# Performance work log

Measured on AMD Instinct MI355X. Metric: run time of the kernel, lower is better.

The kernel has to match this reference:

```python
import jax, jax.numpy as jnp
import numpy as np

N, T, D, H, NH, BS = 4, 4096, 512, 8, 4, 64
DH = D // H                 # head dim = 64
NB = T // BS                # n_buckets = 64
CS = NH * NB                # chunk_size = 256
L = NH * T                  # sorted sequence length per head


def setup_inputs() -> dict:
    key = jax.random.key(0)
    ks = jax.random.split(key, 4)
    x = jax.random.normal(ks[0], (N, T, D), jnp.float32)
    W_Q = jax.random.normal(ks[1], (D, D), jnp.float32) * (D ** -0.5)
    W_V = jax.random.normal(ks[2], (D, D), jnp.float32) * (D ** -0.5)
    b_Q = jnp.zeros((D,), jnp.float32)
    b_V = jnp.zeros((D,), jnp.float32)
    gamma = jnp.ones((D,), jnp.float32)
    beta = jnp.zeros((D,), jnp.float32)
    # per-head random rotations: (dim_head, num_hashes, n_buckets // 2)
    rotations = jax.random.normal(ks[3], (H, DH, NH, NB // 2), jnp.float32)
    return {"x": x, "W_Q": W_Q, "b_Q": b_Q, "W_V": W_V, "b_V": b_V,
            "gamma": gamma, "beta": beta, "rotations": rotations}


def _look_one_back(a):
    # concat each chunk with the previous chunk (wrap-around for chunk 0)
    extra = jnp.concatenate([a[:, -1:], a[:, :-1]], axis=1)
    return jnp.concatenate([a, extra], axis=2)


def _lsh_head(qk, v, rot):
    # qk, v: [N, T, DH]; rot: [DH, NH, NB//2]
    rotated = jnp.einsum('btf,fhi->bhti', qk, rot)               # [N,NH,T,NB//2]
    rotated = jnp.concatenate([rotated, -rotated], axis=-1)       # [N,NH,T,NB]
    buckets = jnp.argmax(rotated, axis=-1)                        # [N,NH,T]
    offsets = (jnp.arange(NH) * NB)[None, :, None]
    buckets = (buckets + offsets).reshape(N, L)                   # [N, NH*T]

    ticker = jnp.broadcast_to(jnp.arange(L)[None, :], (N, L))
    buckets_and_t = T * buckets + (ticker % T)                    # unique keys
    sticker = jnp.argsort(buckets_and_t, axis=-1)                 # sorted ticker ids
    undo_sort = jnp.argsort(sticker, axis=-1)
    st = sticker % T                                              # original positions

    sqk = jnp.take_along_axis(qk, st[..., None], axis=1)          # [N,L,DH]
    sv = jnp.take_along_axis(v, st[..., None], axis=1)

    bq_t = st.reshape(N, CS, -1)                                  # [N,CS,BS]
    bqk = sqk.reshape(N, CS, -1, DH)
    bv = sv.reshape(N, CS, -1, DH)
    bq = bqk
    bk = bqk / (jnp.linalg.norm(bqk, axis=-1, keepdims=True) + 1e-6)

    bk = _look_one_back(bk)                                       # [N,CS,2*BS,DH]
    bv = _look_one_back(bv)
    bkv_t = _look_one_back(bq_t)

    dots = jnp.einsum('bcie,bcje->bcij', bq, bk) * (DH ** -0.5)   # [N,CS,BS,2BS]

    # mask out pairs hashed to different buckets
    q_sb = jnp.take_along_axis(buckets, sticker, axis=1).reshape(N, CS, -1)
    kv_sb = _look_one_back(q_sb)
    dots = jnp.where(q_sb[:, :, :, None] != kv_sb[:, :, None, :], -1e9, dots)
    # down-weight self-attention (same position)
    dots = jnp.where(bq_t[:, :, :, None] == bkv_t[:, :, None, :], -1e-5, dots)

    lse = jax.nn.logsumexp(dots, axis=-1, keepdims=True)
    probs = jnp.exp(dots - lse)
    bo = jnp.einsum('bcij,bcje->bcie', probs, bv)                 # [N,CS,BS,DH]

    so = bo.reshape(N, L, DH)
    slog = lse.reshape(N, L)
    o = jnp.take_along_axis(so, undo_sort[..., None], axis=1)
    logits = jnp.take_along_axis(slog, undo_sort, axis=1)

    o = o.reshape(N, NH, T, DH)
    logits = logits.reshape(N, NH, T, 1)
    pw = jnp.exp(logits - jax.nn.logsumexp(logits, axis=1, keepdims=True))
    return jnp.sum(o * pw, axis=1)                                # [N,T,DH]


def reference(x, W_Q, b_Q, W_V, b_V, gamma, beta, rotations):
    Q = x @ W_Q + b_Q
    V = x @ W_V + b_V
    Qh = Q.reshape(N, T, H, DH).transpose(2, 0, 1, 3)             # [H,N,T,DH]
    Vh = V.reshape(N, T, H, DH).transpose(2, 0, 1, 3)
    outs = jax.vmap(_lsh_head)(Qh, Vh, rotations)                 # [H,N,T,DH]
    out = outs.transpose(1, 2, 0, 3).reshape(N, T, D)
    mu = out.mean(axis=-1, keepdims=True)
    var = out.var(axis=-1, keepdims=True)
    return gamma * (out - mu) / jnp.sqrt(var + 1e-3) + beta
```

## Files before the change

kernel.cpp:

```cpp
#include <hip/hip_runtime.h>
#include <hip/hip_bf16.h>

#define N_ 4
#define T_ 4096
#define D_ 512
#define H_ 8
#define DH_ 64
#define NH_ 4
#define NB_ 64
#define CS_ 256
#define L_ 16384

typedef unsigned short u16;
typedef unsigned int u32;
typedef __attribute__((ext_vector_type(8))) short short8;
typedef __attribute__((ext_vector_type(8))) _Float16 half8;
typedef __attribute__((ext_vector_type(4))) float f32x4;

__device__ __forceinline__ u16 f2bf(float x){
    union { float f; u32 u; } c; c.f = x;
    u32 u = c.u;
    u32 r = (u + 0x7FFFu + ((u >> 16) & 1u)) >> 16;
    return (u16)r;
}
__device__ __forceinline__ float bf2f(u16 b){
    union { u32 u; float f; } c; c.u = ((u32)b) << 16;
    return c.f;
}
__device__ __forceinline__ u16 f2h(float x){
    _Float16 h = (_Float16)x;
    u16 r; __builtin_memcpy(&r, &h, 2); return r;
}

__global__ __launch_bounds__(256) void k_decXf(const float* __restrict__ x,
        u16* __restrict__ xf){
    int i = blockIdx.x * 256 + threadIdx.x;
    float4 v = ((const float4*)x)[i];
    ushort4 o;
    o.x = f2h(v.x); o.y = f2h(v.y); o.z = f2h(v.z); o.w = f2h(v.w);
    ((ushort4*)xf)[i] = o;
}

__global__ __launch_bounds__(256) void k_decWv(const float* __restrict__ Wv,
        u16* __restrict__ wvt){
    __shared__ float tile[32][33];
    const int tid = threadIdx.x;
    const int kt = blockIdx.x * 32, nt = blockIdx.y * 32;
    const int tx = tid & 31, ty = tid >> 5;
    #pragma unroll
    for (int i = 0; i < 4; ++i)
        tile[ty + i * 8][tx] = Wv[(size_t)(kt + ty + i * 8) * 512 + nt + tx];
    __syncthreads();
    #pragma unroll
    for (int i = 0; i < 4; ++i){
        int n = ty + i * 8;
        wvt[(size_t)(nt + n) * 512 + kt + tx] = f2h(tile[tx][n]);
    }
}

__global__ __launch_bounds__(256) void k_q(const float* __restrict__ x,
        const float* __restrict__ Wq, const float* __restrict__ bq,
        float* __restrict__ Q){
    __shared__ float sA[16][132];
    __shared__ float sB[16][68];
    const int tid = threadIdx.x;
    const int tx = tid & 15, ty = tid >> 4;
    const int mb = blockIdx.x * 128, nb = blockIdx.y * 64;
    float acc[8][4] = {};
    for (int k0 = 0; k0 < 512; k0 += 16){
        #pragma unroll
        for (int i = 0; i < 2; ++i){
            int idx = i * 256 + tid;
            int m = idx >> 2, kq = idx & 3;
            float4 v = *(const float4*)&x[(size_t)(mb + m) * 512 + k0 + kq * 4];
            sA[kq * 4 + 0][m] = v.x;
            sA[kq * 4 + 1][m] = v.y;
            sA[kq * 4 + 2][m] = v.z;
            sA[kq * 4 + 3][m] = v.w;
        }
        {
            int kk = tid >> 4, nq = tid & 15;
            *(float4*)&sB[kk][nq * 4] =
                *(const float4*)&Wq[(size_t)(k0 + kk) * 512 + nb + nq * 4];
        }
        __syncthreads();
        #pragma unroll
        for (int kk = 0; kk < 16; ++kk){
            float a[8], b[4];
            *(float4*)&a[0] = *(const float4*)&sA[kk][ty * 8];
            *(float4*)&a[4] = *(const float4*)&sA[kk][ty * 8 + 4];
            *(float4*)&b[0] = *(const float4*)&sB[kk][tx * 4];
            #pragma unroll
            for (int i = 0; i < 8; ++i)
                #pragma unroll
                for (int j = 0; j < 4; ++j) acc[i][j] += a[i] * b[j];
        }
        __syncthreads();
    }
    float4 bi = *(const float4*)&bq[nb + tx * 4];
    #pragma unroll
    for (int i = 0; i < 8; ++i){
        float4 o;
        o.x = acc[i][0] + bi.x; o.y = acc[i][1] + bi.y;
        o.z = acc[i][2] + bi.z; o.w = acc[i][3] + bi.w;
        *(float4*)&Q[(size_t)(mb + ty * 8 + i) * 512 + nb + tx * 4] = o;
    }
}

__global__ __launch_bounds__(256) void k_gemmV(const u16* __restrict__ xf,
        const u16* __restrict__ wvt, const float* __restrict__ bv,
        float* __restrict__ V){
    __shared__ __align__(16) u16 sA[128 * 40];
    __shared__ __align__(16) u16 sB[128 * 40];
    const int tid = threadIdx.x;
    const int mb = blockIdx.x * 128, nb = blockIdx.y * 128;
    const int w = tid >> 6, lane = tid & 63, quad = lane >> 4, cc = lane & 15;
    const int wm = (w & 1) * 64, wn = (w >> 1) * 64;
    f32x4 acc[4][4];
    #pragma unroll
    for (int i = 0; i < 4; ++i)
        #pragma unroll
        for (int j = 0; j < 4; ++j) acc[i][j] = (f32x4){0.f, 0.f, 0.f, 0.f};

    for (int k0 = 0; k0 < 512; k0 += 32){
        #pragma unroll
        for (int i = 0; i < 2; ++i){
            int idx = i * 256 + tid;
            int m = idx >> 2, ks = idx & 3;
            *(short8*)&sA[m * 40 + ks * 8] =
                *(const short8*)&xf[(size_t)(mb + m) * 512 + k0 + ks * 8];
            *(short8*)&sB[m * 40 + ks * 8] =
                *(const short8*)&wvt[(size_t)(nb + m) * 512 + k0 + ks * 8];
        }
        __syncthreads();
        half8 a[4], b[4];
        #pragma unroll
        for (int i = 0; i < 4; ++i){
            a[i] = *(const half8*)&sA[(wm + i * 16 + cc) * 40 + quad * 8];
            b[i] = *(const half8*)&sB[(wn + i * 16 + cc) * 40 + quad * 8];
        }
        #pragma unroll
        for (int i = 0; i < 4; ++i)
            #pragma unroll
            for (int j = 0; j < 4; ++j)
                acc[i][j] = __builtin_amdgcn_mfma_f32_16x16x32_f16(a[i], b[j], acc[i][j], 0, 0, 0);
        __syncthreads();
    }
    #pragma unroll
    for (int i = 0; i < 4; ++i)
        #pragma unroll
        for (int j = 0; j < 4; ++j){
            int c = nb + wn + j * 16 + cc;
            float bi = bv[c];
            #pragma unroll
            for (int r = 0; r < 4; ++r){
                int m = mb + wm + i * 16 + quad * 4 + r;
                V[(size_t)m * 512 + c] = acc[i][j][r] + bi;
            }
        }
}

__global__ __launch_bounds__(256) void k_rot(const float* __restrict__ Q,
        const float* __restrict__ rot, int* __restrict__ buckets){
    const int tb = blockIdx.x * 32;
    const int n = blockIdx.y, h = blockIdx.z;
    const int hn = h * N_ + n;
    __shared__ float Rs[64 * 128];
    __shared__ float Qs[32][64];
    const int tid = threadIdx.x;
    const float* rh = rot + (size_t)h * (64 * 128);
    for (int i = tid; i < 8192; i += 256) Rs[i] = rh[i];
    for (int i = tid; i < 2048; i += 256){
        int t = i >> 6, f = i & 63;
        Qs[t][f] = Q[(size_t)(n * T_ + tb + t) * 512 + h * 64 + f];
    }
    __syncthreads();
    const int tx = tid & 31, tg = tid >> 5;
    float r[4][4] = {};
    for (int f = 0; f < 64; ++f){
        float q0 = Qs[tg * 4 + 0][f], q1 = Qs[tg * 4 + 1][f];
        float q2 = Qs[tg * 4 + 2][f], q3 = Qs[tg * 4 + 3][f];
        #pragma unroll
        for (int jj = 0; jj < 4; ++jj){
            float rv = Rs[f * 128 + jj * 32 + tx];
            r[0][jj] += q0 * rv; r[1][jj] += q1 * rv;
            r[2][jj] += q2 * rv; r[3][jj] += q3 * rv;
        }
    }
    #pragma unroll
    for (int tt = 0; tt < 4; ++tt){
        #pragma unroll
        for (int jj = 0; jj < 4; ++jj){
            float bv = r[tt][jj]; int bi = tx;
            float nv = -bv;
            if (nv > bv){ bv = nv; bi = 32 + tx; }
            #pragma unroll
            for (int m = 16; m >= 1; m >>= 1){
                float ov = __shfl_xor(bv, m, 32);
                int   oi = __shfl_xor(bi, m, 32);
                if (ov > bv || (ov == bv && oi < bi)){ bv = ov; bi = oi; }
            }
            if (tx == 0){
                int t = tb + tg * 4 + tt;
                buckets[(size_t)hn * L_ + jj * T_ + t] = bi + jj * 64;
            }
        }
    }
}

__global__ __launch_bounds__(256) void k_hist(const int* __restrict__ buckets,
        int* __restrict__ hist){
    const int tile = blockIdx.x, hn = blockIdx.y;
    const int tid = threadIdx.x;
    __shared__ int h[256];
    h[tid] = 0;
    __syncthreads();
    int b = buckets[(size_t)hn * L_ + tile * 256 + tid];
    atomicAdd(&h[b], 1);
    __syncthreads();
    hist[((size_t)hn * 64 + tile) * 256 + tid] = h[tid];
}

__global__ __launch_bounds__(256) void k_scan(int* __restrict__ hist,
        int* __restrict__ bucketStart){
    const int hn = blockIdx.x;
    const int b = threadIdx.x;
    int* hh = hist + (size_t)hn * 64 * 256;
    int run = 0;
    for (int tl = 0; tl < 64; ++tl){
        int v = hh[tl * 256 + b];
        hh[tl * 256 + b] = run;
        run += v;
    }
    __shared__ int s[256];
    s[b] = run;
    __syncthreads();
    for (int off = 1; off < 256; off <<= 1){
        int add = (b >= off) ? s[b - off] : 0;
        __syncthreads();
        s[b] += add;
        __syncthreads();
    }
    bucketStart[hn * 256 + b] = s[b] - run;
}

__global__ __launch_bounds__(256) void k_scatter(const int* __restrict__ buckets,
        const int* __restrict__ offs, const int* __restrict__ bucketStart,
        int* __restrict__ sticker){
    const int tile = blockIdx.x, hn = blockIdx.y;
    const int tid = threadIdx.x;
    __shared__ int sb[256];
    const int i = tile * 256 + tid;
    const int b = buckets[(size_t)hn * L_ + i];
    sb[tid] = b;
    __syncthreads();
    int rank = 0;
    #pragma unroll 8
    for (int j = 0; j < 256; ++j){
        int v = sb[j];
        rank += (j < tid && v == b) ? 1 : 0;
    }
    int pos = bucketStart[hn * 256 + b]
            + offs[((size_t)hn * 64 + tile) * 256 + b]
            + rank;
    sticker[(size_t)hn * L_ + pos] = i;
}

__global__ __launch_bounds__(256) void k_attn(const float* __restrict__ Q,
        const float* __restrict__ V, const int* __restrict__ buckets,
        const int* __restrict__ sticker, u16* __restrict__ o_hash,
        float* __restrict__ logit_hash){
    const int blk_c = blockIdx.x, n = blockIdx.y, h = blockIdx.z;
    const int hn = h * N_ + n;
    const int tid = threadIdx.x;
    const int w = tid >> 6, lane = tid & 63;
    const int quad = lane >> 4, cc = lane & 15;

    __shared__ __align__(16) u16 sQ[128 * 64];
    __shared__ __align__(16) u16 sVt[64 * 128];
    __shared__ __align__(16) u16 sP[64 * 128];
    __shared__ int s_idx[128], s_buck[128], s_t[128];
    __shared__ float s_inv[128];
    __shared__ float s_lse[64];

    if (tid < 128){
        int cprev = (blk_c + CS_ - 1) & (CS_ - 1);
        int pos = (tid < 64) ? blk_c * 64 + tid : cprev * 64 + (tid - 64);
        int idx = sticker[(size_t)hn * L_ + pos];
        s_idx[tid] = idx;
        s_buck[tid] = buckets[(size_t)hn * L_ + idx];
        s_t[tid] = idx & (T_ - 1);
    }
    __syncthreads();

    for (int pass = 0; pass < 8; ++pass){
        int r = pass * 16 + w * 4 + quad;
        int t = s_t[r];
        const float4* qp = (const float4*)&Q[(size_t)(n * T_ + t) * 512 + h * 64];
        float4 qv = qp[cc];
        int c0 = cc * 4;
        int physq = ((c0 >> 3) ^ (r & 7));
        u16* dst = &sQ[r * 64 + physq * 8 + (c0 & 7)];
        dst[0] = f2bf(qv.x); dst[1] = f2bf(qv.y);
        dst[2] = f2bf(qv.z); dst[3] = f2bf(qv.w);
        float ss = qv.x * qv.x + qv.y * qv.y + qv.z * qv.z + qv.w * qv.w;
        #pragma unroll
        for (int m = 8; m >= 1; m >>= 1) ss += __shfl_xor(ss, m, 64);
        if (cc == 0) s_inv[r] = 1.f / (sqrtf(ss) + 1e-6f);
        const float4* vp = (const float4*)&V[(size_t)(n * T_ + t) * 512 + h * 64];
        float4 vv = vp[cc];
        float ve[4] = {vv.x, vv.y, vv.z, vv.w};
        #pragma unroll
        for (int i = 0; i < 4; ++i){
            int d = c0 + i;
            sVt[d * 128 + (((r >> 3) ^ (d & 15)) * 8) + (r & 7)] = f2bf(ve[i]);
        }
    }
    __syncthreads();

    f32x4 dacc[8];
    #pragma unroll
    for (int j = 0; j < 8; ++j) dacc[j] = (f32x4){0.f, 0.f, 0.f, 0.f};
    const int qrow = w * 16 + cc;
    #pragma unroll
    for (int kc = 0; kc < 2; ++kc){
        short8 afrag = *(const short8*)&sQ[qrow * 64 + (((kc * 4 + quad) ^ (cc & 7)) * 8)];
        #pragma unroll
        for (int kt = 0; kt < 8; ++kt){
            int krow = kt * 16 + cc;
            short8 bfrag = *(const short8*)&sQ[krow * 64 + (((kc * 4 + quad) ^ (cc & 7)) * 8)];
            dacc[kt] = __builtin_amdgcn_mfma_f32_16x16x32_bf16(afrag, bfrag, dacc[kt], 0, 0, 0);
        }
    }

    int bq[4], tq[4];
    #pragma unroll
    for (int r = 0; r < 4; ++r){
        int q = w * 16 + quad * 4 + r;
        bq[r] = s_buck[q]; tq[r] = s_t[q];
    }
    float mrow[4] = {-1e30f, -1e30f, -1e30f, -1e30f};
    #pragma unroll
    for (int kt = 0; kt < 8; ++kt){
        int kk = kt * 16 + cc;
        float inv = s_inv[kk] * 0.125f;
        int bk = s_buck[kk], tk = s_t[kk];
        #pragma unroll
        for (int r = 0; r < 4; ++r){
            float d = dacc[kt][r] * inv;
            if (bk != bq[r]) d = -1e9f;
            if (tk == tq[r]) d = -1e-5f;
            dacc[kt][r] = d;
            mrow[r] = fmaxf(mrow[r], d);
        }
    }
    #pragma unroll
    for (int r = 0; r < 4; ++r)
        #pragma unroll
        for (int m = 8; m >= 1; m >>= 1)
            mrow[r] = fmaxf(mrow[r], __shfl_xor(mrow[r], m, 64));
    float srow[4] = {0.f, 0.f, 0.f, 0.f};
    #pragma unroll
    for (int kt = 0; kt < 8; ++kt)
        #pragma unroll
        for (int r = 0; r < 4; ++r)
            srow[r] += __expf(dacc[kt][r] - mrow[r]);
    #pragma unroll
    for (int r = 0; r < 4; ++r)
        #pragma unroll
        for (int m = 8; m >= 1; m >>= 1)
            srow[r] += __shfl_xor(srow[r], m, 64);
    float lse[4];
    #pragma unroll
    for (int r = 0; r < 4; ++r) lse[r] = mrow[r] + __logf(srow[r]);
    if (cc == 0){
        #pragma unroll
        for (int r = 0; r < 4; ++r) s_lse[w * 16 + quad * 4 + r] = lse[r];
    }

    #pragma unroll
    for (int kt = 0; kt < 8; ++kt){
        int kk = kt * 16 + cc;
        #pragma unroll
        for (int r = 0; r < 4; ++r){
            int q = w * 16 + quad * 4 + r;
            sP[q * 128 + (((kk >> 3) ^ (q & 15)) * 8) + (kk & 7)] =
                f2bf(__expf(dacc[kt][r] - lse[r]));
        }
    }
    __syncthreads();

    f32x4 oacc[4];
    #pragma unroll
    for (int j = 0; j < 4; ++j) oacc[j] = (f32x4){0.f, 0.f, 0.f, 0.f};
    #pragma unroll
    for (int kc = 0; kc < 4; ++kc){
        short8 afrag = *(const short8*)&sP[qrow * 128 + (((kc * 4 + quad) ^ cc) * 8)];
        #pragma unroll
        for (int nt = 0; nt < 4; ++nt){
            int d = nt * 16 + cc;
            short8 bfrag = *(const short8*)&sVt[d * 128 + (((kc * 4 + quad) ^ cc) * 8)];
            oacc[nt] = __builtin_amdgcn_mfma_f32_16x16x32_bf16(afrag, bfrag, oacc[nt], 0, 0, 0);
        }
    }

    #pragma unroll
    for (int r = 0; r < 4; ++r){
        int q = w * 16 + quad * 4 + r;
        int si = s_idx[q];
        int jj = si >> 12; int t = si & (T_ - 1);
        size_t base = ((size_t)(hn * NH_ + jj) * T_ + t) * 64;
        #pragma unroll
        for (int nt = 0; nt < 4; ++nt)
            o_hash[base + nt * 16 + cc] = f2bf(oacc[nt][r]);
    }
    if (tid < 64){
        int si = s_idx[tid]; int jj = si >> 12; int t = si & (T_ - 1);
        logit_hash[(size_t)(hn * NH_ + jj) * T_ + t] = s_lse[tid];
    }
}

__global__ __launch_bounds__(256) void k_comb(const u16* __restrict__ o_hash,
        const float* __restrict__ logit_hash, const float* __restrict__ gamma,
        const float* __restrict__ beta, float* __restrict__ out){
    const int t = blockIdx.x, n = blockIdx.y;
    const int tid = threadIdx.x;
    __shared__ float s_pw[32];
    __shared__ float s_x[512];
    __shared__ float s_red[8];
    __shared__ float s_mu, s_rs;
    if (tid < 32){
        int h = tid >> 2, j = tid & 3;
        s_pw[tid] = logit_hash[(size_t)((h * N_ + n) * NH_ + j) * T_ + t];
    }
    __syncthreads();
    if (tid < 8){
        int h = tid;
        float m = -1e30f;
        #pragma unroll
        for (int j = 0; j < 4; ++j) m = fmaxf(m, s_pw[h * 4 + j]);
        float l = 0.f;
        #pragma unroll
        for (int j = 0; j < 4; ++j) l += __expf(s_pw[h * 4 + j] - m);
        float ls = m + __logf(l);
        #pragma unroll
        for (int j = 0; j < 4; ++j) s_pw[h * 4 + j] = __expf(s_pw[h * 4 + j] - ls);
    }
    __syncthreads();
    float va[2];
    #pragma unroll
    for (int i = 0; i < 2; ++i){
        int cidx = tid + i * 256;
        int h = cidx >> 6, d = cidx & 63;
        size_t base = (size_t)((h * N_ + n) * NH_) * T_ * 64;
        float acc = 0.f;
        #pragma unroll
        for (int j = 0; j < 4; ++j)
            acc += s_pw[h * 4 + j] * bf2f(o_hash[base + ((size_t)j * T_ + t) * 64 + d]);
        s_x[cidx] = acc; va[i] = acc;
    }
    float s1 = va[0] + va[1];
    float s2 = va[0] * va[0] + va[1] * va[1];
    #pragma unroll
    for (int m = 32; m >= 1; m >>= 1){
        s1 += __shfl_xor(s1, m, 64);
        s2 += __shfl_xor(s2, m, 64);
    }
    const int lane = tid & 63, w = tid >> 6;
    if (lane == 0){ s_red[w] = s1; s_red[4 + w] = s2; }
    __syncthreads();
    if (tid == 0){
        float S1 = s_red[0] + s_red[1] + s_red[2] + s_red[3];
        float S2 = s_red[4] + s_red[5] + s_red[6] + s_red[7];
        float mu = S1 / 512.f;
        float var = S2 / 512.f - mu * mu;
        s_mu = mu; s_rs = 1.f / sqrtf(var + 1e-3f);
    }
    __syncthreads();
    #pragma unroll
    for (int i = 0; i < 2; ++i){
        int cidx = tid + i * 256;
        out[((size_t)(n * T_ + t)) * 512 + cidx] =
            gamma[cidx] * (s_x[cidx] - s_mu) * s_rs + beta[cidx];
    }
}

extern "C" void kernel_launch(void* const* d_in, const int* in_sizes, int n_in,
                              void* d_out, int out_size, void* d_ws, size_t ws_size,
                              hipStream_t stream){
    const float* x     = (const float*)d_in[0];
    const float* Wq    = (const float*)d_in[1];
    const float* bq    = (const float*)d_in[2];
    const float* Wv    = (const float*)d_in[3];
    const float* bv    = (const float*)d_in[4];
    const float* gamma = (const float*)d_in[5];
    const float* beta  = (const float*)d_in[6];
    const float* rot   = (const float*)d_in[7];
    char* ws = (char*)d_ws;
    float* Q        = (float*)(ws + 0);
    float* V        = (float*)(ws + 33554432);
    int*   buckets  = (int*)  (ws + 67108864);
    int*   sticker  = (int*)  (ws + 69206016);
    float* logit    = (float*)(ws + 71303168);
    u16*   o_hash   = (u16*)  (ws + 73400320);
    u16*   xf       = (u16*)  (ws + 73400320);
    u16*   wvt      = (u16*)  (ws + 90177536);
    int*   hist     = (int*)  (ws + 73400320);
    int*   bstart   = (int*)  (ws + 75497472);

    hipLaunchKernelGGL(k_decXf,   dim3(8192),       dim3(256), 0, stream,
                       x, xf);
    hipLaunchKernelGGL(k_decWv,   dim3(16, 16),     dim3(256), 0, stream,
                       Wv, wvt);
    hipLaunchKernelGGL(k_gemmV,   dim3(128, 4),     dim3(256), 0, stream,
                       xf, wvt, bv, V);
    hipLaunchKernelGGL(k_q,       dim3(128, 8),     dim3(256), 0, stream,
                       x, Wq, bq, Q);
    hipLaunchKernelGGL(k_rot,     dim3(128, 4, 8),  dim3(256), 0, stream,
                       Q, rot, buckets);
    hipLaunchKernelGGL(k_hist,    dim3(64, 32),     dim3(256), 0, stream,
                       buckets, hist);
    hipLaunchKernelGGL(k_scan,    dim3(32),         dim3(256), 0, stream,
                       hist, bstart);
    hipLaunchKernelGGL(k_scatter, dim3(64, 32),     dim3(256), 0, stream,
                       buckets, hist, bstart, sticker);
    hipLaunchKernelGGL(k_attn,    dim3(256, 4, 8),  dim3(256), 0, stream,
                       Q, V, buckets, sticker, o_hash, logit);
    hipLaunchKernelGGL(k_comb,    dim3(4096, 4),    dim3(256), 0, stream,
                       o_hash, logit, gamma, beta, (float*)d_out);
}
```

Measured before the change: 458.8 us.

## Precompute head-major bf16 Q/V and row inverse norms before attention

The Q and V GEMM epilogues now also write bf16, head-major copies ([h,n,t,64]), and the Q kernel stores each row's inverse norm. The attention kernel can then gather Q and V rows with 16-byte bf16 loads instead of strided fp32 loads, and it no longer converts or reduces them per chunk. Softmax probabilities reuse the stored exponentials scaled by 1/sum rather than calling exp a second time. The cost is extra global writes and a larger workspace; V is now rounded to bf16 once at the GEMM instead of later.

```diff
diff --git a/kernel.cpp b/kernel.cpp
--- a/kernel.cpp
+++ b/kernel.cpp
@@ -60,12 +60,13 @@
 
 __global__ __launch_bounds__(256) void k_q(const float* __restrict__ x,
         const float* __restrict__ Wq, const float* __restrict__ bq,
-        float* __restrict__ Q){
+        float* __restrict__ Q, u16* __restrict__ Qbf, float* __restrict__ qinv){
     __shared__ float sA[16][132];
     __shared__ float sB[16][68];
     const int tid = threadIdx.x;
     const int tx = tid & 15, ty = tid >> 4;
     const int mb = blockIdx.x * 128, nb = blockIdx.y * 64;
+    const int h = blockIdx.y;
     float acc[8][4] = {};
     for (int k0 = 0; k0 < 512; k0 += 16){
         #pragma unroll
@@ -100,16 +101,26 @@
     float4 bi = *(const float4*)&bq[nb + tx * 4];
     #pragma unroll
     for (int i = 0; i < 8; ++i){
-        float4 o;
-        o.x = acc[i][0] + bi.x; o.y = acc[i][1] + bi.y;
-        o.z = acc[i][2] + bi.z; o.w = acc[i][3] + bi.w;
-        *(float4*)&Q[(size_t)(mb + ty * 8 + i) * 512 + nb + tx * 4] = o;
+        float o0 = acc[i][0] + bi.x, o1 = acc[i][1] + bi.y;
+        float o2 = acc[i][2] + bi.z, o3 = acc[i][3] + bi.w;
+        int m = mb + ty * 8 + i;
+        float4 o4; o4.x = o0; o4.y = o1; o4.z = o2; o4.w = o3;
+        *(float4*)&Q[(size_t)m * 512 + nb + tx * 4] = o4;
+        float ss = o0 * o0 + o1 * o1 + o2 * o2 + o3 * o3;
+        #pragma unroll
+        for (int s = 8; s >= 1; s >>= 1) ss += __shfl_xor(ss, s, 64);
+        int n = m >> 12, t = m & (T_ - 1);
+        size_t rowb = (size_t)(h * N_ + n) * T_ + t;
+        if (tx == 0) qinv[rowb] = 1.f / (sqrtf(ss) + 1e-6f);
+        ushort4 ob;
+        ob.x = f2bf(o0); ob.y = f2bf(o1); ob.z = f2bf(o2); ob.w = f2bf(o3);
+        *(ushort4*)&Qbf[rowb * 64 + tx * 4] = ob;
     }
 }
 
 __global__ __launch_bounds__(256) void k_gemmV(const u16* __restrict__ xf,
         const u16* __restrict__ wvt, const float* __restrict__ bv,
-        float* __restrict__ V){
+        u16* __restrict__ Vbf){
     __shared__ __align__(16) u16 sA[128 * 40];
     __shared__ __align__(16) u16 sB[128 * 40];
     const int tid = threadIdx.x;
@@ -151,11 +162,13 @@
         #pragma unroll
         for (int j = 0; j < 4; ++j){
             int c = nb + wn + j * 16 + cc;
+            int hh = c >> 6, d = c & 63;
             float bi = bv[c];
             #pragma unroll
             for (int r = 0; r < 4; ++r){
                 int m = mb + wm + i * 16 + quad * 4 + r;
-                V[(size_t)m * 512 + c] = acc[i][j][r] + bi;
+                int n = m >> 12, t = m & (T_ - 1);
+                Vbf[((size_t)(hh * N_ + n) * T_ + t) * 64 + d] = f2bf(acc[i][j][r] + bi);
             }
         }
 }
@@ -266,10 +279,10 @@
     sticker[(size_t)hn * L_ + pos] = i;
 }
 
-__global__ __launch_bounds__(256) void k_attn(const float* __restrict__ Q,
-        const float* __restrict__ V, const int* __restrict__ buckets,
-        const int* __restrict__ sticker, u16* __restrict__ o_hash,
-        float* __restrict__ logit_hash){
+__global__ __launch_bounds__(256) void k_attn(const u16* __restrict__ Qbf,
+        const u16* __restrict__ Vbf, const float* __restrict__ qinv,
+        const int* __restrict__ buckets, const int* __restrict__ sticker,
+        u16* __restrict__ o_hash, float* __restrict__ logit_hash){
     const int blk_c = blockIdx.x, n = blockIdx.y, h = blockIdx.z;
     const int hn = h * N_ + n;
     const int tid = threadIdx.x;
@@ -289,31 +302,24 @@
         int idx = sticker[(size_t)hn * L_ + pos];
         s_idx[tid] = idx;
         s_buck[tid] = buckets[(size_t)hn * L_ + idx];
-        s_t[tid] = idx & (T_ - 1);
-    }
-    __syncthreads();
-
-    for (int pass = 0; pass < 8; ++pass){
-        int r = pass * 16 + w * 4 + quad;
-        int t = s_t[r];
-        const float4* qp = (const float4*)&Q[(size_t)(n * T_ + t) * 512 + h * 64];
-        float4 qv = qp[cc];
-        int c0 = cc * 4;
-        int physq = ((c0 >> 3) ^ (r & 7));
-        u16* dst = &sQ[r * 64 + physq * 8 + (c0 & 7)];
-        dst[0] = f2bf(qv.x); dst[1] = f2bf(qv.y);
-        dst[2] = f2bf(qv.z); dst[3] = f2bf(qv.w);
-        float ss = qv.x * qv.x + qv.y * qv.y + qv.z * qv.z + qv.w * qv.w;
-        #pragma unroll
-        for (int m = 8; m >= 1; m >>= 1) ss += __shfl_xor(ss, m, 64);
-        if (cc == 0) s_inv[r] = 1.f / (sqrtf(ss) + 1e-6f);
-        const float4* vp = (const float4*)&V[(size_t)(n * T_ + t) * 512 + h * 64];
-        float4 vv = vp[cc];
-        float ve[4] = {vv.x, vv.y, vv.z, vv.w};
-        #pragma unroll
-        for (int i = 0; i < 4; ++i){
-            int d = c0 + i;
-            sVt[d * 128 + (((r >> 3) ^ (d & 15)) * 8) + (r & 7)] = f2bf(ve[i]);
+        int t = idx & (T_ - 1);
+        s_t[tid] = t;
+        s_inv[tid] = qinv[(size_t)hn * T_ + t];
+    }
+    __syncthreads();
+
+    const int r0 = tid >> 3, l8 = tid & 7;
+    #pragma unroll
+    for (int it = 0; it < 4; ++it){
+        int r = it * 32 + r0;
+        size_t gb = ((size_t)hn * T_ + s_t[r]) * 64 + l8 * 8;
+        short8 qv = *(const short8*)&Qbf[gb];
+        *(short8*)&sQ[r * 64 + ((l8 ^ (r & 7)) * 8)] = qv;
+        short8 vv = *(const short8*)&Vbf[gb];
+        #pragma unroll
+        for (int i = 0; i < 8; ++i){
+            int d = l8 * 8 + i;
+            sVt[d * 128 + (((r >> 3) ^ (d & 15)) * 8) + (r & 7)] = (u16)vv[i];
         }
     }
     __syncthreads();
@@ -363,16 +369,22 @@
     #pragma unroll
     for (int kt = 0; kt < 8; ++kt)
         #pragma unroll
-        for (int r = 0; r < 4; ++r)
-            srow[r] += __expf(dacc[kt][r] - mrow[r]);
+        for (int r = 0; r < 4; ++r){
+            float e = __expf(dacc[kt][r] - mrow[r]);
+            dacc[kt][r] = e;
+            srow[r] += e;
+        }
     #pragma unroll
     for (int r = 0; r < 4; ++r)
         #pragma unroll
         for (int m = 8; m >= 1; m >>= 1)
             srow[r] += __shfl_xor(srow[r], m, 64);
-    float lse[4];
-    #pragma unroll
-    for (int r = 0; r < 4; ++r) lse[r] = mrow[r] + __logf(srow[r]);
+    float lse[4], pscale[4];
+    #pragma unroll
+    for (int r = 0; r < 4; ++r){
+        lse[r] = mrow[r] + __logf(srow[r]);
+        pscale[r] = 1.f / srow[r];
+    }
     if (cc == 0){
         #pragma unroll
         for (int r = 0; r < 4; ++r) s_lse[w * 16 + quad * 4 + r] = lse[r];
@@ -385,7 +397,7 @@
         for (int r = 0; r < 4; ++r){
             int q = w * 16 + quad * 4 + r;
             sP[q * 128 + (((kk >> 3) ^ (q & 15)) * 8) + (kk & 7)] =
-                f2bf(__expf(dacc[kt][r] - lse[r]));
+                f2bf(dacc[kt][r] * pscale[r]);
         }
     }
     __syncthreads();
@@ -498,24 +510,26 @@
     const float* rot   = (const float*)d_in[7];
     char* ws = (char*)d_ws;
     float* Q        = (float*)(ws + 0);
-    float* V        = (float*)(ws + 33554432);
-    int*   buckets  = (int*)  (ws + 67108864);
-    int*   sticker  = (int*)  (ws + 69206016);
-    float* logit    = (float*)(ws + 71303168);
-    u16*   o_hash   = (u16*)  (ws + 73400320);
-    u16*   xf       = (u16*)  (ws + 73400320);
-    u16*   wvt      = (u16*)  (ws + 90177536);
-    int*   hist     = (int*)  (ws + 73400320);
-    int*   bstart   = (int*)  (ws + 75497472);
+    u16*   o_hash   = (u16*)  (ws + 0);
+    u16*   Qbf      = (u16*)  (ws + 67108864);
+    u16*   Vbf      = (u16*)  (ws + 83886080);
+    float* qinv     = (float*)(ws + 100663296);
+    int*   buckets  = (int*)  (ws + 101187584);
+    int*   sticker  = (int*)  (ws + 103284736);
+    float* logit    = (float*)(ws + 105381888);
+    int*   hist     = (int*)  (ws + 107479040);
+    int*   bstart   = (int*)  (ws + 109576192);
+    u16*   xf       = (u16*)  (ws + 109608960);
+    u16*   wvt      = (u16*)  (ws + 126386176);
 
     hipLaunchKernelGGL(k_decXf,   dim3(8192),       dim3(256), 0, stream,
                        x, xf);
     hipLaunchKernelGGL(k_decWv,   dim3(16, 16),     dim3(256), 0, stream,
                        Wv, wvt);
     hipLaunchKernelGGL(k_gemmV,   dim3(128, 4),     dim3(256), 0, stream,
-                       xf, wvt, bv, V);
+                       xf, wvt, bv, Vbf);
     hipLaunchKernelGGL(k_q,       dim3(128, 8),     dim3(256), 0, stream,
-                       x, Wq, bq, Q);
+                       x, Wq, bq, Q, Qbf, qinv);
     hipLaunchKernelGGL(k_rot,     dim3(128, 4, 8),  dim3(256), 0, stream,
                        Q, rot, buckets);
     hipLaunchKernelGGL(k_hist,    dim3(64, 32),     dim3(256), 0, stream,
@@ -525,7 +539,7 @@
     hipLaunchKernelGGL(k_scatter, dim3(64, 32),     dim3(256), 0, stream,
                        buckets, hist, bstart, sticker);
     hipLaunchKernelGGL(k_attn,    dim3(256, 4, 8),  dim3(256), 0, stream,
-                       Q, V, buckets, sticker, o_hash, logit);
+                       Qbf, Vbf, qinv, buckets, sticker, o_hash, logit);
     hipLaunchKernelGGL(k_comb,    dim3(4096, 4),    dim3(256), 0, stream,
                        o_hash, logit, gamma, beta, (float*)d_out);
 }
```

Result: faster. 427.6 us (-6.8%).
